# Performance work log

Hardware: AMD Instinct MI355X
Metric: run time of the kernel (lower is better)

The kernel has to match this reference:

```python
import jax, jax.numpy as jnp
import numpy as np

V, E, H, O = 25000, 300, 512, 1
B, T = 128, 512


def setup_inputs() -> dict:
    key = jax.random.key(0)
    ks = jax.random.split(key, 8)
    # xavier-uniform style init for weight matrices
    def xav(k, shape):
        fan_in, fan_out = shape[1], shape[0]
        lim = jnp.sqrt(6.0 / (fan_in + fan_out)).astype(jnp.float32)
        return jax.random.uniform(k, shape, jnp.float32, -lim, lim)
    x = jax.random.randint(ks[0], (B, T), 0, V)
    h0 = jnp.zeros((1, B, H), jnp.float32)
    c0 = jnp.zeros((1, B, H), jnp.float32)
    emb = jax.random.normal(ks[1], (V, E), jnp.float32)
    W_ih = xav(ks[2], (4 * H, E))
    W_hh = xav(ks[3], (4 * H, H))
    b_ih = jnp.zeros((4 * H,), jnp.float32)
    b_hh = jnp.zeros((4 * H,), jnp.float32)
    fc_w = xav(ks[4], (O, H))
    fc_b = jnp.zeros((O,), jnp.float32)
    return {"x": x, "h0": h0, "c0": c0, "emb": emb, "W_ih": W_ih,
            "W_hh": W_hh, "b_ih": b_ih, "b_hh": b_hh, "fc_w": fc_w, "fc_b": fc_b}


def reference(x, h0, c0, emb, W_ih, W_hh, b_ih, b_hh, fc_w, fc_b):
    # embedding lookup: [B, T, E]
    embed = emb[x]
    # precompute input projections for all timesteps: [T, B, 4H]
    gates_x = jnp.einsum('bte,ge->tbg', embed, W_ih) + b_ih + b_hh

    def step(carry, gx):
        h, c = carry  # [B, H], [B, H]
        gates = gx + h @ W_hh.T  # [B, 4H]
        i, f, g, o = jnp.split(gates, 4, axis=-1)
        i = jax.nn.sigmoid(i)
        f = jax.nn.sigmoid(f)
        g = jnp.tanh(g)
        o = jax.nn.sigmoid(o)
        c = f * c + i * g
        h = o * jnp.tanh(c)
        return (h, c), h

    (h_T, c_T), hs = jax.lax.scan(step, (h0[0], c0[0]), gates_x)
    output = jnp.transpose(hs, (1, 0, 2))[None]  # [1, B, T, H]
    h_out = output[:, :, -1:]                     # [1, B, 1, H]
    c_out = c_T[None]                             # [1, B, H]
    y = h_out @ fc_w.T + fc_b                     # [1, B, 1, O]
    return y, h_out, c_out
```

## Files before the change

### kernel.cpp

```cpp
#include <hip/hip_runtime.h>

#define VOCAB 25000
#define EDIM  300
#define EPAD  320
#define HDIM  512
#define G4    2048
#define BATCH 128
#define TLEN  512
#define NB_J  16
#define JT_W  32
#define NTHR  512

typedef __attribute__((ext_vector_type(8))) short short8;
typedef __attribute__((ext_vector_type(4))) float f32x4;

static __device__ __forceinline__ unsigned short f2bf(float f) {
    unsigned int u = __float_as_uint(f);
    unsigned int r = u + 0x7fffu + ((u >> 16) & 1u);
    return (unsigned short)(r >> 16);
}

__global__ void conv_pad(const float* __restrict__ src, unsigned short* __restrict__ dst,
                         int rows, int cs, int cd) {
    long total = (long)rows * cd;
    for (long i = blockIdx.x * (long)blockDim.x + threadIdx.x; i < total;
         i += (long)gridDim.x * blockDim.x) {
        int r = (int)(i / cd), c = (int)(i % cd);
        dst[i] = (c < cs) ? f2bf(src[(long)r * cs + c]) : (unsigned short)0;
    }
}

__global__ __launch_bounds__(NTHR, 2) void lstm_pers(
    const int* __restrict__ x, const float* __restrict__ h0, const float* __restrict__ c0,
    const float* __restrict__ b_ih, const float* __restrict__ b_hh,
    const unsigned short* __restrict__ embb, const unsigned short* __restrict__ wihb,
    const unsigned short* __restrict__ whhb, unsigned short* __restrict__ hb,
    unsigned int* __restrict__ cnt, float* __restrict__ out) {
    const int tid  = threadIdx.x;
    const int bt   = blockIdx.x & 7;
    const int jt   = blockIdx.x >> 3;
    const int m0   = bt * 16;
    const int lane = tid & 63;
    const int wv   = tid >> 6;
    const int gate = wv >> 1, jsub = wv & 1;
    const int g0   = gate * HDIM + jt * JT_W + jsub * 16;
    const int arow = lane & 15;
    const int kch  = (lane >> 4) * 8;

    const int bl = tid >> 5;
    const int jl = tid & 31;
    const int bg = m0 + bl;
    const int jg = jt * JT_W + jl;

    unsigned int* cnt_g = cnt + bt * 32;

    __shared__ alignas(16) unsigned short h_lds[16 * 520];
    __shared__ alignas(16) unsigned short emb_lds[16 * 328];
    __shared__ int x_lds[16 * TLEN];
    __shared__ float lds_g[4][16][36];

    const int brow = g0 + (lane & 15);
    const unsigned short* whp = whhb + (long)brow * HDIM + kch;
    const unsigned short* wip = wihb + (long)brow * EPAD + kch;
#define LDH(i) short8 wh##i = *(const short8*)(whp + i * 32);
#define LDE(i) short8 wi##i = *(const short8*)(wip + i * 32);
    LDH(0) LDH(1) LDH(2) LDH(3) LDH(4) LDH(5) LDH(6) LDH(7)
    LDH(8) LDH(9) LDH(10) LDH(11) LDH(12) LDH(13) LDH(14) LDH(15)
    LDE(0) LDE(1) LDE(2) LDE(3) LDE(4) LDE(5) LDE(6) LDE(7) LDE(8) LDE(9)
#undef LDH
#undef LDE

    for (int i = tid; i < 16 * TLEN; i += NTHR)
        x_lds[i] = x[(m0 + (i >> 9)) * TLEN + (i & 511)];

    float bsum[4];
#pragma unroll
    for (int g = 0; g < 4; ++g) bsum[g] = b_ih[g * HDIM + jg] + b_hh[g * HDIM + jg];

    float c_reg = c0[bg * HDIM + jg];
    float h_reg = h0[bg * HDIM + jg];
    __hip_atomic_store(&hb[bg * HDIM + jg], f2bf(h_reg),
                       __ATOMIC_RELAXED, __HIP_MEMORY_SCOPE_AGENT);

    __syncthreads();
    if (tid == 0)
        __hip_atomic_fetch_add(cnt_g, 1u, __ATOMIC_RELAXED, __HIP_MEMORY_SCOPE_AGENT);

    for (int t = 0; t < TLEN; ++t) {
        {
            int i0 = tid;
            int row = i0 / 40, cc = i0 - row * 40;
            int tok = x_lds[row * TLEN + t];
            *(short8*)&emb_lds[row * 328 + cc * 8] =
                *(const short8*)(embb + (long)tok * EPAD + cc * 8);
            if (tid < 128) {
                int i1 = tid + NTHR;
                row = i1 / 40; cc = i1 - row * 40;
                tok = x_lds[row * TLEN + t];
                *(short8*)&emb_lds[row * 328 + cc * 8] =
                    *(const short8*)(embb + (long)tok * EPAD + cc * 8);
            }
        }
        if (tid == 0) {
            unsigned target = (unsigned)NB_J * (unsigned)(t + 1);
            while (__hip_atomic_load(cnt_g, __ATOMIC_RELAXED, __HIP_MEMORY_SCOPE_AGENT) < target)
                __builtin_amdgcn_s_sleep(1);
        }
        __syncthreads();
        {
            const unsigned long long* hread =
                (const unsigned long long*)(hb + (t & 1) * (BATCH * HDIM));
#pragma unroll
            for (int k = 0; k < 4; ++k) {
                int u = tid + k * NTHR;
                int row = u >> 7, col8 = u & 127;
                unsigned long long v = __hip_atomic_load(
                    hread + (long)(m0 + row) * 128 + col8,
                    __ATOMIC_RELAXED, __HIP_MEMORY_SCOPE_AGENT);
                *(unsigned long long*)&h_lds[row * 520 + col8 * 4] = v;
            }
        }
        __syncthreads();
        f32x4 ah = {0.f, 0.f, 0.f, 0.f}, ae = {0.f, 0.f, 0.f, 0.f};
        short8 a;
#define MH(i) a = *(const short8*)&h_lds[arow * 520 + kch + i * 32]; \
              ah = __builtin_amdgcn_mfma_f32_16x16x32_bf16(a, wh##i, ah, 0, 0, 0);
#define ME(i) a = *(const short8*)&emb_lds[arow * 328 + kch + i * 32]; \
              ae = __builtin_amdgcn_mfma_f32_16x16x32_bf16(a, wi##i, ae, 0, 0, 0);
        MH(0) MH(1) MH(2) MH(3) MH(4) MH(5) MH(6) MH(7)
        MH(8) MH(9) MH(10) MH(11) MH(12) MH(13) MH(14) MH(15)
        ME(0) ME(1) ME(2) ME(3) ME(4) ME(5) ME(6) ME(7) ME(8) ME(9)
#undef MH
#undef ME
        const int crow = (lane >> 4) * 4;
        const int ccol = jsub * 16 + (lane & 15);
#pragma unroll
        for (int r = 0; r < 4; ++r) lds_g[gate][crow + r][ccol] = ah[r] + ae[r];
        __syncthreads();
        float gi = lds_g[0][bl][jl] + bsum[0];
        float gf = lds_g[1][bl][jl] + bsum[1];
        float gg = lds_g[2][bl][jl] + bsum[2];
        float go = lds_g[3][bl][jl] + bsum[3];
        float si = 1.f / (1.f + __expf(-gi));
        float sf = 1.f / (1.f + __expf(-gf));
        float tg = tanhf(gg);
        float so = 1.f / (1.f + __expf(-go));
        c_reg = sf * c_reg + si * tg;
        h_reg = so * tanhf(c_reg);
        unsigned short* hwrite = hb + ((t + 1) & 1) * (BATCH * HDIM);
        __hip_atomic_store(&hwrite[bg * HDIM + jg], f2bf(h_reg),
                           __ATOMIC_RELAXED, __HIP_MEMORY_SCOPE_AGENT);
        __syncthreads();
        if (tid == 0)
            __hip_atomic_fetch_add(cnt_g, 1u, __ATOMIC_RELAXED, __HIP_MEMORY_SCOPE_AGENT);
    }

    out[BATCH + bg * HDIM + jg] = h_reg;
    out[BATCH + BATCH * HDIM + bg * HDIM + jg] = c_reg;
}

__global__ void fc_k(const float* __restrict__ h, const float* __restrict__ fcw,
                     const float* __restrict__ fcb, float* __restrict__ y) {
    int b = blockIdx.x * 4 + (threadIdx.x >> 6);
    int lane = threadIdx.x & 63;
    float s = 0.f;
#pragma unroll
    for (int j = lane; j < HDIM; j += 64) s += h[b * HDIM + j] * fcw[j];
#pragma unroll
    for (int off = 32; off; off >>= 1) s += __shfl_down(s, off, 64);
    if (lane == 0) y[b] = s + fcb[0];
}

extern "C" void kernel_launch(void* const* d_in, const int* in_sizes, int n_in,
                              void* d_out, int out_size, void* d_ws, size_t ws_size,
                              hipStream_t stream) {
    const int*   x   = (const int*)d_in[0];
    const float* h0  = (const float*)d_in[1];
    const float* c0  = (const float*)d_in[2];
    const float* emb = (const float*)d_in[3];
    const float* Wih = (const float*)d_in[4];
    const float* Whh = (const float*)d_in[5];
    const float* bih = (const float*)d_in[6];
    const float* bhh = (const float*)d_in[7];
    const float* fcw = (const float*)d_in[8];
    const float* fcb = (const float*)d_in[9];
    float* out = (float*)d_out;

    char* ws = (char*)d_ws;
    unsigned short* embb = (unsigned short*)(ws);
    unsigned short* wihb = (unsigned short*)(ws + 16000000);
    unsigned short* whhb = (unsigned short*)(ws + 17310720);
    unsigned short* hb   = (unsigned short*)(ws + 19407872);
    unsigned int*   cnt  = (unsigned int*)(ws + 19670016);

    conv_pad<<<2048, 256, 0, stream>>>(emb, embb, VOCAB, EDIM, EPAD);
    conv_pad<<<512, 256, 0, stream>>>(Wih, wihb, G4, EDIM, EPAD);
    conv_pad<<<512, 256, 0, stream>>>(Whh, whhb, G4, HDIM, HDIM);
    hipMemsetAsync((void*)cnt, 0, 8 * 128, stream);

    void* args[] = {(void*)&x, (void*)&h0, (void*)&c0, (void*)&bih, (void*)&bhh,
                    (void*)&embb, (void*)&wihb, (void*)&whhb, (void*)&hb,
                    (void*)&cnt, (void*)&out};
    hipLaunchCooperativeKernel((void*)lstm_pers, dim3(128), dim3(NTHR), args, 0, stream);

    fc_k<<<32, 256, 0, stream>>>(out + BATCH, fcw, fcb, out);
}
```

Baseline: 1.855 ms.

## Replace counter barrier with step-tagged hidden state and prefetch embeddings

```diff
diff --git a/kernel.cpp b/kernel.cpp
--- a/kernel.cpp
+++ b/kernel.cpp
@@ -4,15 +4,14 @@
 #define EDIM  300
 #define EPAD  320
 #define HDIM  512
-#define G4    2048
 #define BATCH 128
 #define TLEN  512
-#define NB_J  16
-#define JT_W  32
 #define NTHR  512
 
 typedef __attribute__((ext_vector_type(8))) short short8;
 typedef __attribute__((ext_vector_type(4))) float f32x4;
+typedef unsigned int u32;
+typedef unsigned long long u64;
 
 static __device__ __forceinline__ unsigned short f2bf(float f) {
     unsigned int u = __float_as_uint(f);
@@ -20,22 +19,18 @@
     return (unsigned short)(r >> 16);
 }
 
-__global__ void conv_pad(const float* __restrict__ src, unsigned short* __restrict__ dst,
-                         int rows, int cs, int cd) {
-    long total = (long)rows * cd;
-    for (long i = blockIdx.x * (long)blockDim.x + threadIdx.x; i < total;
-         i += (long)gridDim.x * blockDim.x) {
-        int r = (int)(i / cd), c = (int)(i % cd);
-        dst[i] = (c < cs) ? f2bf(src[(long)r * cs + c]) : (unsigned short)0;
-    }
+__global__ void conv_pad_row(const float* __restrict__ src, unsigned short* __restrict__ dst,
+                             int rows, int cs, int cd) {
+    for (int r = blockIdx.x; r < rows; r += gridDim.x)
+        for (int c = threadIdx.x; c < cd; c += blockDim.x)
+            dst[(long)r * cd + c] = (c < cs) ? f2bf(src[(long)r * cs + c]) : (unsigned short)0;
 }
 
 __global__ __launch_bounds__(NTHR, 2) void lstm_pers(
     const int* __restrict__ x, const float* __restrict__ h0, const float* __restrict__ c0,
     const float* __restrict__ b_ih, const float* __restrict__ b_hh,
     const unsigned short* __restrict__ embb, const unsigned short* __restrict__ wihb,
-    const unsigned short* __restrict__ whhb, unsigned short* __restrict__ hb,
-    unsigned int* __restrict__ cnt, float* __restrict__ out) {
+    const unsigned short* __restrict__ whhb, u32* __restrict__ hb, float* __restrict__ out) {
     const int tid  = threadIdx.x;
     const int bt   = blockIdx.x & 7;
     const int jt   = blockIdx.x >> 3;
@@ -43,25 +38,22 @@
     const int lane = tid & 63;
     const int wv   = tid >> 6;
     const int gate = wv >> 1, jsub = wv & 1;
-    const int g0   = gate * HDIM + jt * JT_W + jsub * 16;
-    const int arow = lane & 15;
-    const int kch  = (lane >> 4) * 8;
-
-    const int bl = tid >> 5;
-    const int jl = tid & 31;
-    const int bg = m0 + bl;
-    const int jg = jt * JT_W + jl;
-
-    unsigned int* cnt_g = cnt + bt * 32;
-
-    __shared__ alignas(16) unsigned short h_lds[16 * 520];
-    __shared__ alignas(16) unsigned short emb_lds[16 * 328];
+    const int g0   = gate * HDIM + jt * 32 + jsub * 16;
+    const int r    = lane & 15;
+    const int q    = lane >> 4;
+    const int sw   = r & 7;
+
+    const int bl = tid >> 5, jl = tid & 31;
+    const int bg = m0 + bl, jg = jt * 32 + jl;
+
+    __shared__ alignas(16) unsigned short h_lds[16 * 512];
+    __shared__ alignas(16) unsigned short emb_lds[2][16 * 320];
     __shared__ int x_lds[16 * TLEN];
     __shared__ float lds_g[4][16][36];
 
-    const int brow = g0 + (lane & 15);
-    const unsigned short* whp = whhb + (long)brow * HDIM + kch;
-    const unsigned short* wip = wihb + (long)brow * EPAD + kch;
+    const int brow = g0 + r;
+    const unsigned short* whp = whhb + (long)brow * HDIM + q * 8;
+    const unsigned short* wip = wihb + (long)brow * EPAD + q * 8;
 #define LDH(i) short8 wh##i = *(const short8*)(whp + i * 32);
 #define LDE(i) short8 wi##i = *(const short8*)(wip + i * 32);
     LDH(0) LDH(1) LDH(2) LDH(3) LDH(4) LDH(5) LDH(6) LDH(7)
@@ -73,86 +65,122 @@
     for (int i = tid; i < 16 * TLEN; i += NTHR)
         x_lds[i] = x[(m0 + (i >> 9)) * TLEN + (i & 511)];
 
-    float bsum[4];
-#pragma unroll
-    for (int g = 0; g < 4; ++g) bsum[g] = b_ih[g * HDIM + jg] + b_hh[g * HDIM + jg];
+    const float bsum0 = b_ih[0 * HDIM + jg] + b_hh[0 * HDIM + jg];
+    const float bsum1 = b_ih[1 * HDIM + jg] + b_hh[1 * HDIM + jg];
+    const float bsum2 = b_ih[2 * HDIM + jg] + b_hh[2 * HDIM + jg];
+    const float bsum3 = b_ih[3 * HDIM + jg] + b_hh[3 * HDIM + jg];
 
     float c_reg = c0[bg * HDIM + jg];
     float h_reg = h0[bg * HDIM + jg];
-    __hip_atomic_store(&hb[bg * HDIM + jg], f2bf(h_reg),
+
+    u32* const hb0 = hb;
+    u32* const hb1 = hb + BATCH * HDIM;
+    __hip_atomic_store(hb0 + bg * HDIM + jg, (u32)f2bf(h_reg),
                        __ATOMIC_RELAXED, __HIP_MEMORY_SCOPE_AGENT);
 
+    u32 hoff[8], lofs[8];
+#pragma unroll
+    for (int k = 0; k < 8; ++k) {
+        int u   = tid + k * NTHR;
+        int row = u >> 8, col = u & 255;
+        hoff[k] = (u32)((m0 + row) * 256 + col);
+        int chunk = col >> 2, sub = col & 3;
+        lofs[k] = (u32)(row * 512 + ((chunk ^ (row & 7)) * 4 + sub) * 2);
+    }
+
     __syncthreads();
-    if (tid == 0)
-        __hip_atomic_fetch_add(cnt_g, 1u, __ATOMIC_RELAXED, __HIP_MEMORY_SCOPE_AGENT);
+    {
+        int row = tid / 40, cc = tid - row * 40;
+        int tok = x_lds[row * TLEN];
+        *(short8*)&emb_lds[0][row * 320 + ((cc ^ (row & 7)) * 8)] =
+            *(const short8*)(embb + (long)tok * EPAD + cc * 8);
+        if (tid < 128) {
+            int i1 = tid + NTHR; int row2 = i1 / 40, cc2 = i1 - row2 * 40;
+            int tok2 = x_lds[row2 * TLEN];
+            *(short8*)&emb_lds[0][row2 * 320 + ((cc2 ^ (row2 & 7)) * 8)] =
+                *(const short8*)(embb + (long)tok2 * EPAD + cc2 * 8);
+        }
+    }
+    __syncthreads();
 
     for (int t = 0; t < TLEN; ++t) {
+        const int pb = t & 1;
+        const u64* hsrc = (const u64*)(pb ? hb1 : hb0);
+        u64 hv[8];
+#pragma unroll
+        for (int k = 0; k < 8; ++k)
+            hv[k] = __hip_atomic_load(hsrc + hoff[k], __ATOMIC_RELAXED, __HIP_MEMORY_SCOPE_AGENT);
+
         {
-            int i0 = tid;
-            int row = i0 / 40, cc = i0 - row * 40;
-            int tok = x_lds[row * TLEN + t];
-            *(short8*)&emb_lds[row * 328 + cc * 8] =
+            int tn = (t + 1 < TLEN) ? (t + 1) : (TLEN - 1);
+            unsigned short* ebuf = (unsigned short*)emb_lds[pb ^ 1];
+            int row = tid / 40, cc = tid - row * 40;
+            int tok = x_lds[row * TLEN + tn];
+            *(short8*)&ebuf[row * 320 + ((cc ^ (row & 7)) * 8)] =
                 *(const short8*)(embb + (long)tok * EPAD + cc * 8);
             if (tid < 128) {
-                int i1 = tid + NTHR;
-                row = i1 / 40; cc = i1 - row * 40;
-                tok = x_lds[row * TLEN + t];
-                *(short8*)&emb_lds[row * 328 + cc * 8] =
-                    *(const short8*)(embb + (long)tok * EPAD + cc * 8);
+                int i1 = tid + NTHR; int row2 = i1 / 40, cc2 = i1 - row2 * 40;
+                int tok2 = x_lds[row2 * TLEN + tn];
+                *(short8*)&ebuf[row2 * 320 + ((cc2 ^ (row2 & 7)) * 8)] =
+                    *(const short8*)(embb + (long)tok2 * EPAD + cc2 * 8);
             }
         }
-        if (tid == 0) {
-            unsigned target = (unsigned)NB_J * (unsigned)(t + 1);
-            while (__hip_atomic_load(cnt_g, __ATOMIC_RELAXED, __HIP_MEMORY_SCOPE_AGENT) < target)
-                __builtin_amdgcn_s_sleep(1);
+
+        const unsigned short* ecur = (const unsigned short*)emb_lds[pb];
+        f32x4 ae = {0.f, 0.f, 0.f, 0.f};
+        short8 a;
+#define ME(i) a = *(const short8*)&ecur[r * 320 + (((q + 4 * i) ^ sw) * 8)]; \
+              ae = __builtin_amdgcn_mfma_f32_16x16x32_bf16(a, wi##i, ae, 0, 0, 0);
+        ME(0) ME(1) ME(2) ME(3) ME(4) ME(5) ME(6) ME(7) ME(8) ME(9)
+#undef ME
+
+        const u32 want = (u32)t;
+        while (1) {
+            u32 bad = 0;
+#pragma unroll
+            for (int k = 0; k < 8; ++k)
+                bad |= (((u32)(hv[k] >> 16) & 0xFFFFu) ^ want) | (((u32)(hv[k] >> 48)) ^ want);
+            if (!bad) break;
+#pragma unroll
+            for (int k = 0; k < 8; ++k)
+                hv[k] = __hip_atomic_load(hsrc + hoff[k], __ATOMIC_RELAXED, __HIP_MEMORY_SCOPE_AGENT);
+        }
+
+#pragma unroll
+        for (int k = 0; k < 8; ++k) {
+            u32 two = ((u32)hv[k] & 0xFFFFu) | (((u32)(hv[k] >> 32) & 0xFFFFu) << 16);
+            *(u32*)&h_lds[lofs[k]] = two;
         }
         __syncthreads();
-        {
-            const unsigned long long* hread =
-                (const unsigned long long*)(hb + (t & 1) * (BATCH * HDIM));
-#pragma unroll
-            for (int k = 0; k < 4; ++k) {
-                int u = tid + k * NTHR;
-                int row = u >> 7, col8 = u & 127;
-                unsigned long long v = __hip_atomic_load(
-                    hread + (long)(m0 + row) * 128 + col8,
-                    __ATOMIC_RELAXED, __HIP_MEMORY_SCOPE_AGENT);
-                *(unsigned long long*)&h_lds[row * 520 + col8 * 4] = v;
-            }
-        }
-        __syncthreads();
-        f32x4 ah = {0.f, 0.f, 0.f, 0.f}, ae = {0.f, 0.f, 0.f, 0.f};
-        short8 a;
-#define MH(i) a = *(const short8*)&h_lds[arow * 520 + kch + i * 32]; \
+
+        f32x4 ah = {0.f, 0.f, 0.f, 0.f};
+#define MH(i) a = *(const short8*)&h_lds[r * 512 + (((q + 4 * i) ^ sw) * 8)]; \
               ah = __builtin_amdgcn_mfma_f32_16x16x32_bf16(a, wh##i, ah, 0, 0, 0);
-#define ME(i) a = *(const short8*)&emb_lds[arow * 328 + kch + i * 32]; \
-              ae = __builtin_amdgcn_mfma_f32_16x16x32_bf16(a, wi##i, ae, 0, 0, 0);
         MH(0) MH(1) MH(2) MH(3) MH(4) MH(5) MH(6) MH(7)
         MH(8) MH(9) MH(10) MH(11) MH(12) MH(13) MH(14) MH(15)
-        ME(0) ME(1) ME(2) ME(3) ME(4) ME(5) ME(6) ME(7) ME(8) ME(9)
 #undef MH
-#undef ME
-        const int crow = (lane >> 4) * 4;
-        const int ccol = jsub * 16 + (lane & 15);
-#pragma unroll
-        for (int r = 0; r < 4; ++r) lds_g[gate][crow + r][ccol] = ah[r] + ae[r];
+
+        const int crow = q * 4;
+        const int ccol = jsub * 16 + r;
+#pragma unroll
+        for (int rr = 0; rr < 4; ++rr) lds_g[gate][crow + rr][ccol] = ah[rr] + ae[rr];
         __syncthreads();
-        float gi = lds_g[0][bl][jl] + bsum[0];
-        float gf = lds_g[1][bl][jl] + bsum[1];
-        float gg = lds_g[2][bl][jl] + bsum[2];
-        float go = lds_g[3][bl][jl] + bsum[3];
+
+        float gi = lds_g[0][bl][jl] + bsum0;
+        float gf = lds_g[1][bl][jl] + bsum1;
+        float gg = lds_g[2][bl][jl] + bsum2;
+        float go = lds_g[3][bl][jl] + bsum3;
         float si = 1.f / (1.f + __expf(-gi));
         float sf = 1.f / (1.f + __expf(-gf));
-        float tg = tanhf(gg);
+        float tg = 2.f / (1.f + __expf(-2.f * gg)) - 1.f;
         float so = 1.f / (1.f + __expf(-go));
         c_reg = sf * c_reg + si * tg;
-        h_reg = so * tanhf(c_reg);
-        unsigned short* hwrite = hb + ((t + 1) & 1) * (BATCH * HDIM);
-        __hip_atomic_store(&hwrite[bg * HDIM + jg], f2bf(h_reg),
+        float th = 2.f / (1.f + __expf(-2.f * c_reg)) - 1.f;
+        h_reg = so * th;
+        u32* dst = (pb ? hb0 : hb1) + bg * HDIM + jg;
+        __hip_atomic_store(dst, ((u32)(t + 1) << 16) | (u32)f2bf(h_reg),
                            __ATOMIC_RELAXED, __HIP_MEMORY_SCOPE_AGENT);
         __syncthreads();
-        if (tid == 0)
-            __hip_atomic_fetch_add(cnt_g, 1u, __ATOMIC_RELAXED, __HIP_MEMORY_SCOPE_AGENT);
     }
 
     out[BATCH + bg * HDIM + jg] = h_reg;
@@ -190,17 +218,14 @@
     unsigned short* embb = (unsigned short*)(ws);
     unsigned short* wihb = (unsigned short*)(ws + 16000000);
     unsigned short* whhb = (unsigned short*)(ws + 17310720);
-    unsigned short* hb   = (unsigned short*)(ws + 19407872);
-    unsigned int*   cnt  = (unsigned int*)(ws + 19670016);
-
-    conv_pad<<<2048, 256, 0, stream>>>(emb, embb, VOCAB, EDIM, EPAD);
-    conv_pad<<<512, 256, 0, stream>>>(Wih, wihb, G4, EDIM, EPAD);
-    conv_pad<<<512, 256, 0, stream>>>(Whh, whhb, G4, HDIM, HDIM);
-    hipMemsetAsync((void*)cnt, 0, 8 * 128, stream);
+    u32*            hb   = (u32*)(ws + 19407872);
+
+    conv_pad_row<<<4096, 256, 0, stream>>>(emb, embb, VOCAB, EDIM, EPAD);
+    conv_pad_row<<<2048, 256, 0, stream>>>(Wih, wihb, 4 * HDIM, EDIM, EPAD);
+    conv_pad_row<<<2048, 256, 0, stream>>>(Whh, whhb, 4 * HDIM, HDIM, HDIM);
 
     void* args[] = {(void*)&x, (void*)&h0, (void*)&c0, (void*)&bih, (void*)&bhh,
-                    (void*)&embb, (void*)&wihb, (void*)&whhb, (void*)&hb,
-                    (void*)&cnt, (void*)&out};
+                    (void*)&embb, (void*)&wihb, (void*)&whhb, (void*)&hb, (void*)&out};
     hipLaunchCooperativeKernel((void*)lstm_pers, dim3(128), dim3(NTHR), args, 0, stream);
 
     fc_k<<<32, 256, 0, stream>>>(out + BATCH, fcw, fcb, out);
```

New measurement: 1.607 ms. -13.4%, faster.
